# Kernel optimization log

Measured on AMD Instinct MI355X. Metric: run time of the kernel, lower is better.

The kernel has to match this reference:

```python
import jax, jax.numpy as jnp
import numpy as np

jax.config.update("jax_enable_x64", True)  # hash math needs int64 (prime * coord > 2^31)

LEVEL = 16
MOD_T = 2 ** 16
FDIM = 3
_PRIMES = (1, 2654435761, 805459861)  # first feature_dim primes from the module


def _grid_sizes():
    # mirrors torch float32 computation: b = exp((log(n_max)-log(n_min))/(level-1))
    n_min = np.float32(4.0)
    n_max = np.float32(256.0)
    b = np.float32(np.exp((np.log(n_max) - np.log(n_min)) / np.float32(LEVEL - 1)))
    return [int(n_min * b ** i) for i in range(LEVEL)]


def setup_inputs() -> dict:
    key = jax.random.key(0)
    k1, k2 = jax.random.split(key)
    images = jax.random.uniform(k1, (16, 3, 256, 256), dtype=jnp.float32)
    hash_table = (jax.random.uniform(k2, (LEVEL, MOD_T, FDIM), dtype=jnp.float32)
                  * 0.0002 - 0.0001)
    return {"images": images, "hash_table": hash_table}


def reference(images, hash_table):
    b, c, h, w = images.shape
    primes = jnp.array(_PRIMES[:FDIM], dtype=jnp.int64)
    neg_inf = jnp.array(-jnp.inf, dtype=images.dtype)
    outs = []
    for lvl, grid in enumerate(_grid_sizes()):
        kh, kw = h // grid, w // grid
        # max_pool2d(images*grid, kernel=(kh,kw), stride=(kh,kw))
        pooled = jax.lax.reduce_window(
            images * grid, neg_inf, jax.lax.max,
            window_dimensions=(1, 1, kh, kw),
            window_strides=(1, 1, kh, kw),
            padding="VALID")                     # [B, F, gh, gw]
        idx = pooled.astype(jnp.int64) * primes[None, :, None, None]
        g = idx[:, 0]
        for i in range(1, FDIM):
            g = g ^ idx[:, i]
        g = g % MOD_T                             # [B, gh, gw]
        f = hash_table[lvl][g]                    # gather -> [B, gh, gw, F]
        f = jnp.transpose(f, (0, 3, 1, 2))        # [B, F, gh, gw]
        # F.interpolate(..., mode='bilinear') == half-pixel, align_corners=False
        f = jax.image.resize(f, (b, FDIM, h, w), method="bilinear")
        outs.append(f)
    return jnp.concatenate(outs, axis=1)          # [B, level*F, H, W]
```

## Files before the change

kernel.cpp:

```cpp
#include <hip/hip_runtime.h>
#include <stdint.h>
#include <math.h>


#define NLVL 16
#define NB   16

__constant__ int   c_P[NLVL]   = {4,5,6,9,12,15,21,28,36,51,64,85,128,256,256,256};
__constant__ float c_G[NLVL]   = {4.f,5.f,6.f,9.f,12.f,15.f,21.f,27.f,36.f,48.f,63.f,84.f,111.f,147.f,194.f,255.f};
__constant__ int   c_CUM[14]   = {0,16,41,77,158,302,527,968,1752,3048,5649,9745,16970,33354};

#define CELLS_PB   33354
#define CELLS_TOT  (CELLS_PB*NB)
#define MWS_FLOATS (CELLS_TOT*3)
#define POOL_BLOCKS (NB*32)
#define DIR_BLOCKS  1024
#define K1_BLOCKS   (POOL_BLOCKS + DIR_BLOCKS)
#define TILE_BLOCKS (13*16*16)

__device__ __forceinline__ uint32_t hash3(float m0, float m1, float m2, float g) {
    uint32_t v0 = (uint32_t)(int)(m0 * g);
    uint32_t v1 = (uint32_t)(int)(m1 * g);
    uint32_t v2 = (uint32_t)(int)(m2 * g);
    return (v0 ^ (v1 * 2654435761u) ^ (v2 * 805459861u)) & 0xFFFFu;
}

__global__ __launch_bounds__(256) void pool_direct(const float* __restrict__ img,
                                                   const float* __restrict__ tab,
                                                   unsigned int* __restrict__ mws,
                                                   float* __restrict__ out)
{
    static constexpr int K_P[13]   = {4,5,6,9,12,15,21,28,36,51,64,85,128};
    static constexpr int K_KH[13]  = {64,51,42,28,21,17,12,9,7,5,4,3,2};
    static constexpr int K_CUM[13] = {0,16,41,77,158,302,527,968,1752,3048,5649,9745,16970};

    __shared__ float simg[3][8][256];
    __shared__ float colbuf[3][256];

    if (blockIdx.x >= POOL_BLOCKS) {
        int t = (blockIdx.x - POOL_BLOCKS) * 256 + threadIdx.x;
        int b = t >> 14;
        int pix0 = (t & 16383) << 2;
        const float* p = img + (size_t)b * 196608 + pix0;
        float4 i0 = *(const float4*)p;
        float4 i1 = *(const float4*)(p + 65536);
        float4 i2 = *(const float4*)(p + 131072);
#pragma unroll
        for (int lvl = 13; lvl < 16; ++lvl) {
            float g = c_G[lvl];
            const float* T = tab + (size_t)lvl * 196608;
            uint32_t g0 = hash3(i0.x, i1.x, i2.x, g);
            uint32_t g1 = hash3(i0.y, i1.y, i2.y, g);
            uint32_t g2 = hash3(i0.z, i1.z, i2.z, g);
            uint32_t g3 = hash3(i0.w, i1.w, i2.w, g);
            float3 f0 = *(const float3*)(T + g0 * 3);
            float3 f1 = *(const float3*)(T + g1 * 3);
            float3 f2 = *(const float3*)(T + g2 * 3);
            float3 f3 = *(const float3*)(T + g3 * 3);
            float4 o0, o1, o2;
            o0.x = f0.x; o1.x = f0.y; o2.x = f0.z;
            o0.y = f1.x; o1.y = f1.y; o2.y = f1.z;
            o0.z = f2.x; o1.z = f2.y; o2.z = f2.z;
            o0.w = f3.x; o1.w = f3.y; o2.w = f3.z;
            float* ob = out + ((size_t)b * 48 + 3 * lvl) * 65536 + pix0;
            *(float4*)ob            = o0;
            *(float4*)(ob + 65536)  = o1;
            *(float4*)(ob + 131072) = o2;
        }
        return;
    }

    int b    = blockIdx.x >> 5;
    int band = blockIdx.x & 31;
    int y0   = band * 8;

    const float* base = img + (size_t)b * 196608 + (size_t)y0 * 256;
    for (int t = threadIdx.x; t < 1536; t += 256) {
        int ch = t >> 9;
        int r  = t & 511;
        float4 v = *(const float4*)(base + (size_t)ch * 65536 + r * 4);
        int row = r >> 6, c4 = (r & 63) << 2;
        simg[ch][row][c4 + 0] = v.x;
        simg[ch][row][c4 + 1] = v.y;
        simg[ch][row][c4 + 2] = v.z;
        simg[ch][row][c4 + 3] = v.w;
    }
    __syncthreads();

    int x = threadIdx.x;
#pragma unroll
    for (int lvl = 0; lvl < 13; ++lvl) {
        const int kh = K_KH[lvl], P = K_P[lvl];
        int nr0 = y0 / kh;
        int nr1 = (y0 + 7) / kh; if (nr1 > P - 1) nr1 = P - 1;
        for (int cr = nr0; cr <= nr1; ++cr) {
            int rlo = cr * kh;      if (rlo < y0) rlo = y0;
            int rhi = cr * kh + kh; if (rhi > y0 + 8) rhi = y0 + 8;
            float p0 = -INFINITY, p1 = -INFINITY, p2 = -INFINITY;
            for (int r = rlo; r < rhi; ++r) {
                int rr = r - y0;
                p0 = fmaxf(p0, simg[0][rr][x]);
                p1 = fmaxf(p1, simg[1][rr][x]);
                p2 = fmaxf(p2, simg[2][rr][x]);
            }
            colbuf[0][x] = p0; colbuf[1][x] = p1; colbuf[2][x] = p2;
            __syncthreads();
            if (x < P) {
                float q0 = -INFINITY, q1 = -INFINITY, q2 = -INFINITY;
                for (int c = x * kh; c < x * kh + kh; ++c) {
                    q0 = fmaxf(q0, colbuf[0][c]);
                    q1 = fmaxf(q1, colbuf[1][c]);
                    q2 = fmaxf(q2, colbuf[2][c]);
                }
                int idx = K_CUM[lvl] * NB + b * P * P + cr * P + x;
                atomicMax(&mws[idx],                 __float_as_uint(q0));
                atomicMax(&mws[idx + CELLS_TOT],     __float_as_uint(q1));
                atomicMax(&mws[idx + 2 * CELLS_TOT], __float_as_uint(q2));
            }
            __syncthreads();
        }
    }
}

__global__ __launch_bounds__(256) void render_tiles(const float* __restrict__ tab,
                                                    const float* __restrict__ mws,
                                                    float* __restrict__ out)
{
    __shared__ float4 s[34 * 34];
    int blk   = blockIdx.x;
    int tile  = blk & 15;
    int plane = blk >> 4;
    int lvl   = plane >> 4;
    int b     = plane & 15;
    int P     = c_P[lvl];
    int yt0   = (tile >> 2) * 64;
    int xt0   = (tile & 3) * 64;

    int nlo  = ((2 * yt0 + 1) * P - 256) >> 9;
    int r_lo = nlo < 0 ? 0 : (nlo > P - 1 ? P - 1 : nlo);
    int nhi  = (((2 * (yt0 + 63) + 1) * P - 256) >> 9) + 1;
    int r_hi = nhi < 0 ? 0 : (nhi > P - 1 ? P - 1 : nhi);
    int mlo  = ((2 * xt0 + 1) * P - 256) >> 9;
    int c_lo = mlo < 0 ? 0 : (mlo > P - 1 ? P - 1 : mlo);
    int mhi  = (((2 * (xt0 + 63) + 1) * P - 256) >> 9) + 1;
    int c_hi = mhi < 0 ? 0 : (mhi > P - 1 ? P - 1 : mhi);
    int span_y = r_hi - r_lo + 1;
    int span_x = c_hi - c_lo + 1;

    int planebase = c_CUM[lvl] * NB + b * P * P;
    const float* T = tab + (size_t)lvl * 196608;
    float gmul = c_G[lvl];
    int n = span_y * span_x;
    for (int t = threadIdx.x; t < n; t += 256) {
        int r = t / span_x, c = t - r * span_x;
        int idx = planebase + (r_lo + r) * P + c_lo + c;
        float m0 = mws[idx];
        float m1 = mws[idx + CELLS_TOT];
        float m2 = mws[idx + 2 * CELLS_TOT];
        uint32_t g = hash3(m0, m1, m2, gmul);
        float3 tv = *(const float3*)(T + g * 3);
        float4 fv; fv.x = tv.x; fv.y = tv.y; fv.z = tv.z; fv.w = 0.f;
        s[t] = fv;
    }
    __syncthreads();

    int lane = threadIdx.x & 63;
    int w    = threadIdx.x >> 6;
    int xq   = lane & 15;
    int rg   = lane >> 4;
    int xb   = xt0 + xq * 4;

    int ix0t[4], ix1t[4]; float wx1t[4];
#pragma unroll
    for (int j = 0; j < 4; ++j) {
        int numx = (2 * (xb + j) + 1) * P - 256;
        int ix0  = numx >> 9;
        float fx = (float)(numx & 511) * (1.0f / 512.0f);
        int ix1;
        if (ix0 < 0)           { ix0 = 0;     ix1 = 0;     fx = 0.f; }
        else if (ix0 >= P - 1) { ix0 = P - 1; ix1 = P - 1; fx = 0.f; }
        else                   { ix1 = ix0 + 1; }
        ix0t[j] = ix0 - c_lo; ix1t[j] = ix1 - c_lo; wx1t[j] = fx;
    }

#pragma unroll
    for (int k = 0; k < 4; ++k) {
        int y = yt0 + w * 16 + rg * 4 + k;
        int numy = (2 * y + 1) * P - 256;
        int iy0  = numy >> 9;
        float fy = (float)(numy & 511) * (1.0f / 512.0f);
        int iy1;
        if (iy0 < 0)           { iy0 = 0;     iy1 = 0;     fy = 0.f; }
        else if (iy0 >= P - 1) { iy0 = P - 1; iy1 = P - 1; fy = 0.f; }
        else                   { iy1 = iy0 + 1; }
        const float4* p0 = s + (iy0 - r_lo) * span_x;
        const float4* p1 = s + (iy1 - r_lo) * span_x;
        float wy1 = fy, wy0 = 1.f - fy;

        float v[3][4];
#pragma unroll
        for (int j = 0; j < 4; ++j) {
            float wx1 = wx1t[j], wx0 = 1.f - wx1;
            float4 t00 = p0[ix0t[j]];
            float4 t01 = p0[ix1t[j]];
            float4 t10 = p1[ix0t[j]];
            float4 t11 = p1[ix1t[j]];
            v[0][j] = wy0 * (wx0 * t00.x + wx1 * t01.x) + wy1 * (wx0 * t10.x + wx1 * t11.x);
            v[1][j] = wy0 * (wx0 * t00.y + wx1 * t01.y) + wy1 * (wx0 * t10.y + wx1 * t11.y);
            v[2][j] = wy0 * (wx0 * t00.z + wx1 * t01.z) + wy1 * (wx0 * t10.z + wx1 * t11.z);
        }
        float* o = out + ((size_t)b * 48 + 3 * lvl) * 65536 + (size_t)y * 256 + xb;
#pragma unroll
        for (int c = 0; c < 3; ++c) {
            float4 q; q.x = v[c][0]; q.y = v[c][1]; q.z = v[c][2]; q.w = v[c][3];
            *(float4*)(o + (size_t)c * 65536) = q;
        }
    }
}

extern "C" void kernel_launch(void* const* d_in, const int* in_sizes, int n_in,
                              void* d_out, int out_size, void* d_ws, size_t ws_size,
                              hipStream_t stream)
{
    const float* img = (const float*)d_in[0];
    const float* tab = (const float*)d_in[1];
    float* out = (float*)d_out;
    float* mws = (float*)d_ws;

    (void)hipMemsetAsync(mws, 0, (size_t)MWS_FLOATS * sizeof(float), stream);
    hipLaunchKernelGGL(pool_direct,  dim3(K1_BLOCKS), dim3(256), 0, stream, img, tab, (unsigned int*)mws, out);
    hipLaunchKernelGGL(render_tiles, dim3(TILE_BLOCKS), dim3(256), 0, stream, tab, mws, out);
}
```

Before: 76.16 us.

## Fuse pooling, hashing and rendering for levels 10-12 into first kernel

Levels 10-12 are now handled by extra blocks in the first kernel. Each of these blocks max-pools its tile's cells straight from the image, hashes them, gathers the table entries into shared memory and renders the bilinear output, so these levels no longer go through the workspace and the second kernel. The banded pooling loop now covers only levels 0-9, and the render kernel only 10 levels. In exchange, the first kernel needs an extra 18KB of shared memory, which can lower its occupancy, and the fused blocks re-read overlapping image windows without coalescing.

```diff
diff --git a/kernel.cpp b/kernel.cpp
--- a/kernel.cpp
+++ b/kernel.cpp
@@ -7,6 +7,7 @@
 #define NB   16
 
 __constant__ int   c_P[NLVL]   = {4,5,6,9,12,15,21,28,36,51,64,85,128,256,256,256};
+__constant__ int   c_KH[NLVL]  = {64,51,42,28,21,17,12,9,7,5,4,3,2,1,1,1};
 __constant__ float c_G[NLVL]   = {4.f,5.f,6.f,9.f,12.f,15.f,21.f,27.f,36.f,48.f,63.f,84.f,111.f,147.f,194.f,255.f};
 __constant__ int   c_CUM[14]   = {0,16,41,77,158,302,527,968,1752,3048,5649,9745,16970,33354};
 
@@ -15,8 +16,9 @@
 #define MWS_FLOATS (CELLS_TOT*3)
 #define POOL_BLOCKS (NB*32)
 #define DIR_BLOCKS  1024
-#define K1_BLOCKS   (POOL_BLOCKS + DIR_BLOCKS)
-#define TILE_BLOCKS (13*16*16)
+#define T12_BLOCKS  (3*16*16)
+#define K1_BLOCKS   (POOL_BLOCKS + DIR_BLOCKS + T12_BLOCKS)
+#define TILE_BLOCKS (10*16*16)
 
 __device__ __forceinline__ uint32_t hash3(float m0, float m1, float m2, float g) {
     uint32_t v0 = (uint32_t)(int)(m0 * g);
@@ -25,17 +27,129 @@
     return (v0 ^ (v1 * 2654435761u) ^ (v2 * 805459861u)) & 0xFFFFu;
 }
 
-__global__ __launch_bounds__(256) void pool_direct(const float* __restrict__ img,
-                                                   const float* __restrict__ tab,
-                                                   unsigned int* __restrict__ mws,
-                                                   float* __restrict__ out)
-{
-    static constexpr int K_P[13]   = {4,5,6,9,12,15,21,28,36,51,64,85,128};
-    static constexpr int K_KH[13]  = {64,51,42,28,21,17,12,9,7,5,4,3,2};
-    static constexpr int K_CUM[13] = {0,16,41,77,158,302,527,968,1752,3048,5649,9745,16970};
-
+__device__ __forceinline__ void tile_body(const float4* s, int r_lo, int c_lo,
+                                          int span_x, int P, int lvl, int b,
+                                          int yt0, int xt0, float* __restrict__ out)
+{
+    int lane = threadIdx.x & 63;
+    int w    = threadIdx.x >> 6;
+    int xq   = lane & 15;
+    int rg   = lane >> 4;
+    int xb   = xt0 + xq * 4;
+
+    int ix0t[4], ix1t[4]; float wx1t[4];
+#pragma unroll
+    for (int j = 0; j < 4; ++j) {
+        int numx = (2 * (xb + j) + 1) * P - 256;
+        int ix0  = numx >> 9;
+        float fx = (float)(numx & 511) * (1.0f / 512.0f);
+        int ix1;
+        if (ix0 < 0)           { ix0 = 0;     ix1 = 0;     fx = 0.f; }
+        else if (ix0 >= P - 1) { ix0 = P - 1; ix1 = P - 1; fx = 0.f; }
+        else                   { ix1 = ix0 + 1; }
+        ix0t[j] = ix0 - c_lo; ix1t[j] = ix1 - c_lo; wx1t[j] = fx;
+    }
+
+#pragma unroll
+    for (int k = 0; k < 4; ++k) {
+        int y = yt0 + w * 16 + rg * 4 + k;
+        int numy = (2 * y + 1) * P - 256;
+        int iy0  = numy >> 9;
+        float fy = (float)(numy & 511) * (1.0f / 512.0f);
+        int iy1;
+        if (iy0 < 0)           { iy0 = 0;     iy1 = 0;     fy = 0.f; }
+        else if (iy0 >= P - 1) { iy0 = P - 1; iy1 = P - 1; fy = 0.f; }
+        else                   { iy1 = iy0 + 1; }
+        const float4* p0 = s + (iy0 - r_lo) * span_x;
+        const float4* p1 = s + (iy1 - r_lo) * span_x;
+        float wy1 = fy, wy0 = 1.f - fy;
+
+        float v[3][4];
+#pragma unroll
+        for (int j = 0; j < 4; ++j) {
+            float wx1 = wx1t[j], wx0 = 1.f - wx1;
+            float4 t00 = p0[ix0t[j]];
+            float4 t01 = p0[ix1t[j]];
+            float4 t10 = p1[ix0t[j]];
+            float4 t11 = p1[ix1t[j]];
+            v[0][j] = wy0 * (wx0 * t00.x + wx1 * t01.x) + wy1 * (wx0 * t10.x + wx1 * t11.x);
+            v[1][j] = wy0 * (wx0 * t00.y + wx1 * t01.y) + wy1 * (wx0 * t10.y + wx1 * t11.y);
+            v[2][j] = wy0 * (wx0 * t00.z + wx1 * t01.z) + wy1 * (wx0 * t10.z + wx1 * t11.z);
+        }
+        float* o = out + ((size_t)b * 48 + 3 * lvl) * 65536 + (size_t)y * 256 + xb;
+#pragma unroll
+        for (int c = 0; c < 3; ++c) {
+            float4 q; q.x = v[c][0]; q.y = v[c][1]; q.z = v[c][2]; q.w = v[c][3];
+            *(float4*)(o + (size_t)c * 65536) = q;
+        }
+    }
+}
+
+__device__ __forceinline__ void tile_window(int P, int yt0, int xt0,
+                                            int& r_lo, int& c_lo, int& span_y, int& span_x)
+{
+    int nlo  = ((2 * yt0 + 1) * P - 256) >> 9;
+    r_lo = nlo < 0 ? 0 : (nlo > P - 1 ? P - 1 : nlo);
+    int nhi  = (((2 * (yt0 + 63) + 1) * P - 256) >> 9) + 1;
+    int r_hi = nhi < 0 ? 0 : (nhi > P - 1 ? P - 1 : nhi);
+    int mlo  = ((2 * xt0 + 1) * P - 256) >> 9;
+    c_lo = mlo < 0 ? 0 : (mlo > P - 1 ? P - 1 : mlo);
+    int mhi  = (((2 * (xt0 + 63) + 1) * P - 256) >> 9) + 1;
+    int c_hi = mhi < 0 ? 0 : (mhi > P - 1 ? P - 1 : mhi);
+    span_y = r_hi - r_lo + 1;
+    span_x = c_hi - c_lo + 1;
+}
+
+__global__ __launch_bounds__(256) void k1_fused(const float* __restrict__ img,
+                                                const float* __restrict__ tab,
+                                                unsigned int* __restrict__ mws,
+                                                float* __restrict__ out)
+{
+    static constexpr int K_P[10]   = {4,5,6,9,12,15,21,28,36,51};
+    static constexpr int K_KH[10]  = {64,51,42,28,21,17,12,9,7,5};
+    static constexpr int K_CUM[10] = {0,16,41,77,158,302,527,968,1752,3048};
+
+    __shared__ float4 sbuf[34 * 34];
     __shared__ float simg[3][8][256];
     __shared__ float colbuf[3][256];
+
+    if (blockIdx.x >= POOL_BLOCKS + DIR_BLOCKS) {
+        int blk2  = blockIdx.x - (POOL_BLOCKS + DIR_BLOCKS);
+        int lvl   = 10 + (blk2 >> 8);
+        int rem   = blk2 & 255;
+        int b     = rem >> 4;
+        int tile  = rem & 15;
+        int P     = c_P[lvl], kh = c_KH[lvl];
+        int yt0   = (tile >> 2) * 64;
+        int xt0   = (tile & 3) * 64;
+
+        int r_lo, c_lo, span_y, span_x;
+        tile_window(P, yt0, xt0, r_lo, c_lo, span_y, span_x);
+
+        const float* T = tab + (size_t)lvl * 196608;
+        const float* ib = img + (size_t)b * 196608;
+        float gmul = c_G[lvl];
+        int n = span_y * span_x;
+        for (int t = threadIdx.x; t < n; t += 256) {
+            int r = t / span_x, c = t - r * span_x;
+            const float* ip = ib + (size_t)(r_lo + r) * kh * 256 + (c_lo + c) * kh;
+            float m0 = -INFINITY, m1 = -INFINITY, m2 = -INFINITY;
+            for (int rr = 0; rr < kh; ++rr)
+                for (int cc = 0; cc < kh; ++cc) {
+                    int o = rr * 256 + cc;
+                    m0 = fmaxf(m0, ip[o]);
+                    m1 = fmaxf(m1, ip[65536 + o]);
+                    m2 = fmaxf(m2, ip[131072 + o]);
+                }
+            uint32_t g = hash3(m0, m1, m2, gmul);
+            float3 tv = *(const float3*)(T + g * 3);
+            float4 fv; fv.x = tv.x; fv.y = tv.y; fv.z = tv.z; fv.w = 0.f;
+            sbuf[t] = fv;
+        }
+        __syncthreads();
+        tile_body(sbuf, r_lo, c_lo, span_x, P, lvl, b, yt0, xt0, out);
+        return;
+    }
 
     if (blockIdx.x >= POOL_BLOCKS) {
         int t = (blockIdx.x - POOL_BLOCKS) * 256 + threadIdx.x;
@@ -89,7 +203,7 @@
 
     int x = threadIdx.x;
 #pragma unroll
-    for (int lvl = 0; lvl < 13; ++lvl) {
+    for (int lvl = 0; lvl < 10; ++lvl) {
         const int kh = K_KH[lvl], P = K_P[lvl];
         int nr0 = y0 / kh;
         int nr1 = (y0 + 7) / kh; if (nr1 > P - 1) nr1 = P - 1;
@@ -136,16 +250,8 @@
     int yt0   = (tile >> 2) * 64;
     int xt0   = (tile & 3) * 64;
 
-    int nlo  = ((2 * yt0 + 1) * P - 256) >> 9;
-    int r_lo = nlo < 0 ? 0 : (nlo > P - 1 ? P - 1 : nlo);
-    int nhi  = (((2 * (yt0 + 63) + 1) * P - 256) >> 9) + 1;
-    int r_hi = nhi < 0 ? 0 : (nhi > P - 1 ? P - 1 : nhi);
-    int mlo  = ((2 * xt0 + 1) * P - 256) >> 9;
-    int c_lo = mlo < 0 ? 0 : (mlo > P - 1 ? P - 1 : mlo);
-    int mhi  = (((2 * (xt0 + 63) + 1) * P - 256) >> 9) + 1;
-    int c_hi = mhi < 0 ? 0 : (mhi > P - 1 ? P - 1 : mhi);
-    int span_y = r_hi - r_lo + 1;
-    int span_x = c_hi - c_lo + 1;
+    int r_lo, c_lo, span_y, span_x;
+    tile_window(P, yt0, xt0, r_lo, c_lo, span_y, span_x);
 
     int planebase = c_CUM[lvl] * NB + b * P * P;
     const float* T = tab + (size_t)lvl * 196608;
@@ -163,59 +269,7 @@
         s[t] = fv;
     }
     __syncthreads();
-
-    int lane = threadIdx.x & 63;
-    int w    = threadIdx.x >> 6;
-    int xq   = lane & 15;
-    int rg   = lane >> 4;
-    int xb   = xt0 + xq * 4;
-
-    int ix0t[4], ix1t[4]; float wx1t[4];
-#pragma unroll
-    for (int j = 0; j < 4; ++j) {
-        int numx = (2 * (xb + j) + 1) * P - 256;
-        int ix0  = numx >> 9;
-        float fx = (float)(numx & 511) * (1.0f / 512.0f);
-        int ix1;
-        if (ix0 < 0)           { ix0 = 0;     ix1 = 0;     fx = 0.f; }
-        else if (ix0 >= P - 1) { ix0 = P - 1; ix1 = P - 1; fx = 0.f; }
-        else                   { ix1 = ix0 + 1; }
-        ix0t[j] = ix0 - c_lo; ix1t[j] = ix1 - c_lo; wx1t[j] = fx;
-    }
-
-#pragma unroll
-    for (int k = 0; k < 4; ++k) {
-        int y = yt0 + w * 16 + rg * 4 + k;
-        int numy = (2 * y + 1) * P - 256;
-        int iy0  = numy >> 9;
-        float fy = (float)(numy & 511) * (1.0f / 512.0f);
-        int iy1;
-        if (iy0 < 0)           { iy0 = 0;     iy1 = 0;     fy = 0.f; }
-        else if (iy0 >= P - 1) { iy0 = P - 1; iy1 = P - 1; fy = 0.f; }
-        else                   { iy1 = iy0 + 1; }
-        const float4* p0 = s + (iy0 - r_lo) * span_x;
-        const float4* p1 = s + (iy1 - r_lo) * span_x;
-        float wy1 = fy, wy0 = 1.f - fy;
-
-        float v[3][4];
-#pragma unroll
-        for (int j = 0; j < 4; ++j) {
-            float wx1 = wx1t[j], wx0 = 1.f - wx1;
-            float4 t00 = p0[ix0t[j]];
-            float4 t01 = p0[ix1t[j]];
-            float4 t10 = p1[ix0t[j]];
-            float4 t11 = p1[ix1t[j]];
-            v[0][j] = wy0 * (wx0 * t00.x + wx1 * t01.x) + wy1 * (wx0 * t10.x + wx1 * t11.x);
-            v[1][j] = wy0 * (wx0 * t00.y + wx1 * t01.y) + wy1 * (wx0 * t10.y + wx1 * t11.y);
-            v[2][j] = wy0 * (wx0 * t00.z + wx1 * t01.z) + wy1 * (wx0 * t10.z + wx1 * t11.z);
-        }
-        float* o = out + ((size_t)b * 48 + 3 * lvl) * 65536 + (size_t)y * 256 + xb;
-#pragma unroll
-        for (int c = 0; c < 3; ++c) {
-            float4 q; q.x = v[c][0]; q.y = v[c][1]; q.z = v[c][2]; q.w = v[c][3];
-            *(float4*)(o + (size_t)c * 65536) = q;
-        }
-    }
+    tile_body(s, r_lo, c_lo, span_x, P, lvl, b, yt0, xt0, out);
 }
 
 extern "C" void kernel_launch(void* const* d_in, const int* in_sizes, int n_in,
@@ -228,6 +282,6 @@
     float* mws = (float*)d_ws;
 
     (void)hipMemsetAsync(mws, 0, (size_t)MWS_FLOATS * sizeof(float), stream);
-    hipLaunchKernelGGL(pool_direct,  dim3(K1_BLOCKS), dim3(256), 0, stream, img, tab, (unsigned int*)mws, out);
+    hipLaunchKernelGGL(k1_fused,     dim3(K1_BLOCKS), dim3(256), 0, stream, img, tab, (unsigned int*)mws, out);
     hipLaunchKernelGGL(render_tiles, dim3(TILE_BLOCKS), dim3(256), 0, stream, tab, mws, out);
 }
```

New measurement: 78.69 us. 1.03x slower.
